# Kernel tuning notes

Measured on AMD Instinct MI355X. Metric: run time of the kernel, lower is better.

The kernel has to match this reference:

```python
import jax, jax.numpy as jnp
import numpy as np

N_NODES = 100000

def _sage_conv(x, src, dst, w_l, b_l, w_r):
    # PyG SAGEConv (mean aggr): out = lin_l(mean_j x_j) + lin_r(x_i)
    msg = x[src]                                             # [E, d] gather
    agg = jax.ops.segment_sum(msg, dst, num_segments=N_NODES)
    deg = jax.ops.segment_sum(jnp.ones((src.shape[0],), x.dtype), dst,
                              num_segments=N_NODES)
    mean = agg / jnp.maximum(deg, 1.0)[:, None]
    return mean @ w_l.T + b_l + x @ w_r.T


def setup_inputs() -> dict:
    key = jax.random.key(0)
    ks = jax.random.split(key, 9)
    d_in, d_h, d_out = 128, 128, 4
    E = 1600000
    x = jax.random.normal(ks[0], (N_NODES, d_in), dtype=jnp.float32)
    edge_index = jax.random.randint(ks[1], (2, E), 0, N_NODES, dtype=jnp.int32)
    s = lambda k, shp, fan: jax.random.normal(k, shp, jnp.float32) / np.sqrt(fan)
    return {
        "x": x,
        "edge_index": edge_index,
        "w1_l": s(ks[2], (d_h, d_in), d_in),
        "b1_l": jnp.zeros((d_h,), jnp.float32),
        "w1_r": s(ks[3], (d_h, d_in), d_in),
        "w2_l": s(ks[4], (d_h, d_h), d_h),
        "b2_l": jnp.zeros((d_h,), jnp.float32),
        "w2_r": s(ks[5], (d_h, d_h), d_h),
        "w_out": s(ks[6], (d_out, d_h), d_h),
        "b_out": jnp.zeros((d_out,), jnp.float32),
    }


def reference(x, edge_index, w1_l, b1_l, w1_r, w2_l, b2_l, w2_r, w_out, b_out):
    src, dst = edge_index[0], edge_index[1]
    h = jax.nn.relu(_sage_conv(x, src, dst, w1_l, b1_l, w1_r))
    h = jax.nn.relu(_sage_conv(h, src, dst, w2_l, b2_l, w2_r))
    return h @ w_out.T + b_out
```

## Files before the change

kernel.cpp:

```cpp
#include <hip/hip_runtime.h>

constexpr int D = 128;
constexpr int BSHIFT = 9;
constexpr int BNODES = 1 << BSHIFT;
constexpr int NBUCK_MAX = 256;
using short8 = __attribute__((ext_vector_type(8))) short;
using f32x4  = __attribute__((ext_vector_type(4))) float;

__device__ __forceinline__ unsigned rneb(float f) {
    unsigned u = __float_as_uint(f);
    return (u + 0x7fffu + ((u >> 16) & 1u)) >> 16;
}
__device__ __forceinline__ float lo2f(unsigned u) { return __uint_as_float(u << 16); }
__device__ __forceinline__ float hi2f(unsigned u) { return __uint_as_float(u & 0xffff0000u); }

__global__ __launch_bounds__(256) void misc_kernel(
    const float* __restrict__ w1l, const float* __restrict__ w1r,
    const float* __restrict__ w2l, const float* __restrict__ w2r,
    unsigned short* __restrict__ wf,
    const float* __restrict__ x, unsigned short* __restrict__ xb, int n4,
    int* __restrict__ bcnt)
{
    if (blockIdx.x < 32) {
        int t = blockIdx.x * 256 + threadIdx.x;
        int m = t >> 11;
        int r = t & 2047;
        int f = r >> 6, lane = r & 63;
        int c = f >> 2, ks = f & 3;
        int col = c * 16 + (lane & 15);
        int k0 = ks * 32 + (lane >> 4) * 8;
        const float* W = (m == 0) ? w1l : (m == 1) ? w1r : (m == 2) ? w2l : w2r;
        unsigned short o[8];
#pragma unroll
        for (int i = 0; i < 8; ++i) o[i] = (unsigned short)rneb(W[col * D + k0 + i]);
        uint4 pk;
        pk.x = o[0] | ((unsigned)o[1] << 16);
        pk.y = o[2] | ((unsigned)o[3] << 16);
        pk.z = o[4] | ((unsigned)o[5] << 16);
        pk.w = o[6] | ((unsigned)o[7] << 16);
        reinterpret_cast<uint4*>(wf)[t] = pk;
        return;
    }
    if (blockIdx.x == 32) bcnt[threadIdx.x] = 0;
    int i = (blockIdx.x - 32) * 256 + threadIdx.x;
    if (i >= n4) return;
    float4 v = reinterpret_cast<const float4*>(x)[i];
    uint2 o;
    o.x = rneb(v.x) | (rneb(v.y) << 16);
    o.y = rneb(v.z) | (rneb(v.w) << 16);
    reinterpret_cast<uint2*>(xb)[i] = o;
}

__global__ __launch_bounds__(256) void bucket_count(
    const int* __restrict__ dstI, int* __restrict__ bcnt, int E, int nb)
{
    __shared__ int lh[NBUCK_MAX];
    const int t = threadIdx.x;
    const int e0 = blockIdx.x * 4096;
    for (int i = t; i < nb; i += 256) lh[i] = 0;
    __syncthreads();
#pragma unroll
    for (int q = 0; q < 16; ++q) {
        int e = e0 + q * 256 + t;
        if (e < E) atomicAdd(&lh[dstI[e] >> BSHIFT], 1);
    }
    __syncthreads();
    for (int b = t; b < nb; b += 256)
        if (lh[b] > 0) atomicAdd(&bcnt[b], lh[b]);
}

__global__ __launch_bounds__(256) void bucket_scan(
    const int* __restrict__ bcnt, int* __restrict__ bbase,
    int* __restrict__ gcursor, int nb)
{
    __shared__ int tmp[256];
    const int t = threadIdx.x;
    const int v = (t < nb) ? bcnt[t] : 0;
    tmp[t] = v;
    __syncthreads();
    for (int off = 1; off < 256; off <<= 1) {
        int u = (t >= off) ? tmp[t - off] : 0;
        __syncthreads();
        tmp[t] += u;
        __syncthreads();
    }
    int excl = tmp[t] - v;
    if (t < nb) { bbase[t] = excl; gcursor[t] = excl; }
    if (t == nb - 1) bbase[nb] = excl + v;
}

__global__ __launch_bounds__(256) void bin_kernel(
    const int* __restrict__ srcI, const int* __restrict__ dstI,
    int* __restrict__ gcursor, unsigned* __restrict__ binned, int E, int nb)
{
    __shared__ int lhist[NBUCK_MAX];
    __shared__ int lbase[NBUCK_MAX];
    __shared__ int lcnt[NBUCK_MAX];
    const int t = threadIdx.x;
    const int e0 = blockIdx.x * 4096;
    for (int i = t; i < nb; i += 256) { lhist[i] = 0; lcnt[i] = 0; }
    __syncthreads();

    int dcache[16], scache[16];
#pragma unroll
    for (int q = 0; q < 16; ++q) {
        int e = e0 + q * 256 + t;
        int d = (e < E) ? dstI[e] : -1;
        dcache[q] = d;
        scache[q] = (e < E) ? srcI[e] : 0;
        if (d >= 0) atomicAdd(&lhist[d >> BSHIFT], 1);
    }
    __syncthreads();
    for (int b = t; b < nb; b += 256)
        if (lhist[b] > 0) lbase[b] = atomicAdd(&gcursor[b], lhist[b]);
    __syncthreads();
#pragma unroll
    for (int q = 0; q < 16; ++q) {
        int d = dcache[q];
        if (d >= 0) {
            int b = d >> BSHIFT;
            int off = atomicAdd(&lcnt[b], 1);
            binned[lbase[b] + off] =
                (unsigned)scache[q] | ((unsigned)(d & (BNODES - 1)) << 17);
        }
    }
}

__global__ __launch_bounds__(256) void bucket_build(
    const unsigned* __restrict__ binned, const int* __restrict__ bbase,
    int* __restrict__ rowptr, int* __restrict__ sorted_src, int n, int E)
{
    __shared__ int hist[BNODES];
    __shared__ int cur[BNODES];
    __shared__ int tmp[256];
    const int t = threadIdx.x;
    const int b = blockIdx.x;
    const int node0 = b << BSHIFT;
    const int ebeg = bbase[b];
    const int eend = bbase[b + 1];

    hist[t] = 0; hist[t + 256] = 0;
    __syncthreads();
    for (int e = ebeg + t; e < eend; e += 256)
        atomicAdd(&hist[(binned[e] >> 17) & (BNODES - 1)], 1);
    __syncthreads();

    const int v0 = hist[2 * t], v1 = hist[2 * t + 1];
    const int s = v0 + v1;
    tmp[t] = s;
    __syncthreads();
    for (int off = 1; off < 256; off <<= 1) {
        int u = (t >= off) ? tmp[t - off] : 0;
        __syncthreads();
        tmp[t] += u;
        __syncthreads();
    }
    const int pre = ebeg + tmp[t] - s;
    const int i0 = node0 + 2 * t, i1 = i0 + 1;
    cur[2 * t] = pre;
    cur[2 * t + 1] = pre + v0;
    if (i0 < n) rowptr[i0] = pre;
    if (i1 < n) rowptr[i1] = pre + v0;
    if (b == 0 && t == 0) rowptr[n] = E;
    __syncthreads();

    for (int e = ebeg + t; e < eend; e += 256) {
        unsigned w = binned[e];
        int pos = atomicAdd(&cur[(w >> 17) & (BNODES - 1)], 1);
        sorted_src[pos] = (int)(w & 0x1FFFF);
    }
}

__global__ __launch_bounds__(256) void aggregate_bf16(
    const unsigned short* __restrict__ feat, const int* __restrict__ sorted_src,
    const int* __restrict__ rowptr, unsigned short* __restrict__ outb, int n)
{
    const int wid = (blockIdx.x * 256 + threadIdx.x) >> 6;
    if (wid >= n) return;
    const int lane = threadIdx.x & 63;
    const int sub = lane >> 4;
    const int part = lane & 15;
    const int beg = rowptr[wid];
    const int end = rowptr[wid + 1];
    const int deg = end - beg;

    float acc[8];
#pragma unroll
    for (int j = 0; j < 8; ++j) acc[j] = 0.f;

    int e = beg;
    for (; e + 16 <= end; e += 16) {
        const int s0 = sorted_src[e + sub];
        const int s1 = sorted_src[e + 4 + sub];
        const int s2 = sorted_src[e + 8 + sub];
        const int s3 = sorted_src[e + 12 + sub];
        const uint4 v0 = *reinterpret_cast<const uint4*>(feat + (size_t)s0 * D + part * 8);
        const uint4 v1 = *reinterpret_cast<const uint4*>(feat + (size_t)s1 * D + part * 8);
        const uint4 v2 = *reinterpret_cast<const uint4*>(feat + (size_t)s2 * D + part * 8);
        const uint4 v3 = *reinterpret_cast<const uint4*>(feat + (size_t)s3 * D + part * 8);
        acc[0] += lo2f(v0.x); acc[1] += hi2f(v0.x);
        acc[2] += lo2f(v0.y); acc[3] += hi2f(v0.y);
        acc[4] += lo2f(v0.z); acc[5] += hi2f(v0.z);
        acc[6] += lo2f(v0.w); acc[7] += hi2f(v0.w);
        acc[0] += lo2f(v1.x); acc[1] += hi2f(v1.x);
        acc[2] += lo2f(v1.y); acc[3] += hi2f(v1.y);
        acc[4] += lo2f(v1.z); acc[5] += hi2f(v1.z);
        acc[6] += lo2f(v1.w); acc[7] += hi2f(v1.w);
        acc[0] += lo2f(v2.x); acc[1] += hi2f(v2.x);
        acc[2] += lo2f(v2.y); acc[3] += hi2f(v2.y);
        acc[4] += lo2f(v2.z); acc[5] += hi2f(v2.z);
        acc[6] += lo2f(v2.w); acc[7] += hi2f(v2.w);
        acc[0] += lo2f(v3.x); acc[1] += hi2f(v3.x);
        acc[2] += lo2f(v3.y); acc[3] += hi2f(v3.y);
        acc[4] += lo2f(v3.z); acc[5] += hi2f(v3.z);
        acc[6] += lo2f(v3.w); acc[7] += hi2f(v3.w);
    }
    if (e + 8 <= end) {
        const int s0 = sorted_src[e + sub];
        const int s1 = sorted_src[e + 4 + sub];
        const uint4 v0 = *reinterpret_cast<const uint4*>(feat + (size_t)s0 * D + part * 8);
        const uint4 v1 = *reinterpret_cast<const uint4*>(feat + (size_t)s1 * D + part * 8);
        acc[0] += lo2f(v0.x); acc[1] += hi2f(v0.x);
        acc[2] += lo2f(v0.y); acc[3] += hi2f(v0.y);
        acc[4] += lo2f(v0.z); acc[5] += hi2f(v0.z);
        acc[6] += lo2f(v0.w); acc[7] += hi2f(v0.w);
        acc[0] += lo2f(v1.x); acc[1] += hi2f(v1.x);
        acc[2] += lo2f(v1.y); acc[3] += hi2f(v1.y);
        acc[4] += lo2f(v1.z); acc[5] += hi2f(v1.z);
        acc[6] += lo2f(v1.w); acc[7] += hi2f(v1.w);
        e += 8;
    }
    if (e + 4 <= end) {
        const int s0 = sorted_src[e + sub];
        const uint4 v0 = *reinterpret_cast<const uint4*>(feat + (size_t)s0 * D + part * 8);
        acc[0] += lo2f(v0.x); acc[1] += hi2f(v0.x);
        acc[2] += lo2f(v0.y); acc[3] += hi2f(v0.y);
        acc[4] += lo2f(v0.z); acc[5] += hi2f(v0.z);
        acc[6] += lo2f(v0.w); acc[7] += hi2f(v0.w);
        e += 4;
    }
    if (e < end) {
        const int ei = e + sub;
        const bool act = ei < end;
        const int s = act ? sorted_src[ei] : sorted_src[beg];
        const float m = act ? 1.f : 0.f;
        const uint4 v = *reinterpret_cast<const uint4*>(feat + (size_t)s * D + part * 8);
        acc[0] += m * lo2f(v.x); acc[1] += m * hi2f(v.x);
        acc[2] += m * lo2f(v.y); acc[3] += m * hi2f(v.y);
        acc[4] += m * lo2f(v.z); acc[5] += m * hi2f(v.z);
        acc[6] += m * lo2f(v.w); acc[7] += m * hi2f(v.w);
    }

#pragma unroll
    for (int j = 0; j < 8; ++j) {
        acc[j] += __shfl_xor(acc[j], 16);
        acc[j] += __shfl_xor(acc[j], 32);
    }

    if (sub == 0) {
        const float inv = (deg > 0) ? 1.0f / (float)deg : 0.f;
        uint4 pk;
        pk.x = rneb(acc[0] * inv) | (rneb(acc[1] * inv) << 16);
        pk.y = rneb(acc[2] * inv) | (rneb(acc[3] * inv) << 16);
        pk.z = rneb(acc[4] * inv) | (rneb(acc[5] * inv) << 16);
        pk.w = rneb(acc[6] * inv) | (rneb(acc[7] * inv) << 16);
        *reinterpret_cast<uint4*>(outb + (size_t)wid * D + part * 8) = pk;
    }
}

__global__ __launch_bounds__(256) void mfma_gemm(
    const unsigned short* __restrict__ aMean, const unsigned short* __restrict__ aSelf,
    const unsigned short* __restrict__ wfL, const unsigned short* __restrict__ wfR,
    const float* __restrict__ bL, unsigned short* __restrict__ outb, int n)
{
    const int lane = threadIdx.x & 63;
    const int wave = threadIdx.x >> 6;
    const int lo = lane & 15, hi = lane >> 4;
    const int row0 = blockIdx.x * 64 + wave * 16;
    int arow = row0 + lo;
    if (arow > n - 1) arow = n - 1;
    const size_t abase = (size_t)arow * D;

    f32x4 acc[8];
#pragma unroll
    for (int c = 0; c < 8; ++c) acc[c] = (f32x4){0.f, 0.f, 0.f, 0.f};

#pragma unroll
    for (int p = 0; p < 2; ++p) {
        const unsigned short* A  = p ? aSelf : aMean;
        const unsigned short* WF = p ? wfR : wfL;
#pragma unroll
        for (int ks = 0; ks < 4; ++ks) {
            short8 af = *reinterpret_cast<const short8*>(A + abase + ks * 32 + hi * 8);
#pragma unroll
            for (int c = 0; c < 8; ++c) {
                short8 bf = *reinterpret_cast<const short8*>(
                    WF + ((((c << 2) | ks) * 64 + lane) << 3));
                acc[c] = __builtin_amdgcn_mfma_f32_16x16x32_bf16(af, bf, acc[c], 0, 0, 0);
            }
        }
    }

#pragma unroll
    for (int c = 0; c < 8; ++c) {
        const int col = (c << 4) | lo;
        const float bias = bL[col];
#pragma unroll
        for (int j = 0; j < 4; ++j) {
            const int row = row0 + (hi << 2) + j;
            if (row < n)
                outb[(size_t)row * D + col] =
                    (unsigned short)rneb(fmaxf(acc[c][j] + bias, 0.f));
        }
    }
}

__global__ __launch_bounds__(256) void mfma_gemm_out(
    const unsigned short* __restrict__ aMean, const unsigned short* __restrict__ aSelf,
    const unsigned short* __restrict__ wfL, const unsigned short* __restrict__ wfR,
    const float* __restrict__ bL, const float* __restrict__ w_out,
    const float* __restrict__ b_out, float* __restrict__ outp, int n)
{
    __shared__ float wsm[4 * D];
    wsm[threadIdx.x] = w_out[threadIdx.x];
    wsm[threadIdx.x + 256] = w_out[threadIdx.x + 256];
    __syncthreads();

    const int lane = threadIdx.x & 63;
    const int wave = threadIdx.x >> 6;
    const int lo = lane & 15, hi = lane >> 4;
    const int row0 = blockIdx.x * 64 + wave * 16;
    int arow = row0 + lo;
    if (arow > n - 1) arow = n - 1;
    const size_t abase = (size_t)arow * D;

    f32x4 acc[8];
#pragma unroll
    for (int c = 0; c < 8; ++c) acc[c] = (f32x4){0.f, 0.f, 0.f, 0.f};

#pragma unroll
    for (int p = 0; p < 2; ++p) {
        const unsigned short* A  = p ? aSelf : aMean;
        const unsigned short* WF = p ? wfR : wfL;
#pragma unroll
        for (int ks = 0; ks < 4; ++ks) {
            short8 af = *reinterpret_cast<const short8*>(A + abase + ks * 32 + hi * 8);
#pragma unroll
            for (int c = 0; c < 8; ++c) {
                short8 bf = *reinterpret_cast<const short8*>(
                    WF + ((((c << 2) | ks) * 64 + lane) << 3));
                acc[c] = __builtin_amdgcn_mfma_f32_16x16x32_bf16(af, bf, acc[c], 0, 0, 0);
            }
        }
    }

    float part[4][4];
#pragma unroll
    for (int j = 0; j < 4; ++j)
#pragma unroll
        for (int d = 0; d < 4; ++d) part[j][d] = 0.f;

#pragma unroll
    for (int c = 0; c < 8; ++c) {
        const int col = (c << 4) | lo;
        const float bias = bL[col];
        const float w0 = wsm[0 * D + col];
        const float w1 = wsm[1 * D + col];
        const float w2 = wsm[2 * D + col];
        const float w3 = wsm[3 * D + col];
#pragma unroll
        for (int j = 0; j < 4; ++j) {
            const float h = fmaxf(acc[c][j] + bias, 0.f);
            part[j][0] += h * w0;
            part[j][1] += h * w1;
            part[j][2] += h * w2;
            part[j][3] += h * w3;
        }
    }

#pragma unroll
    for (int m = 1; m < 16; m <<= 1) {
#pragma unroll
        for (int j = 0; j < 4; ++j)
#pragma unroll
            for (int d = 0; d < 4; ++d)
                part[j][d] += __shfl_xor(part[j][d], m);
    }

    if (lo == 0) {
        const float4 bo = *reinterpret_cast<const float4*>(b_out);
#pragma unroll
        for (int j = 0; j < 4; ++j) {
            const int row = row0 + (hi << 2) + j;
            if (row < n) {
                float4 o;
                o.x = part[j][0] + bo.x;
                o.y = part[j][1] + bo.y;
                o.z = part[j][2] + bo.z;
                o.w = part[j][3] + bo.w;
                *reinterpret_cast<float4*>(outp + (size_t)row * 4) = o;
            }
        }
    }
}

extern "C" void kernel_launch(void* const* d_in, const int* in_sizes, int n_in,
                              void* d_out, int out_size, void* d_ws, size_t ws_size,
                              hipStream_t stream)
{
    const float* x    = (const float*)d_in[0];
    const int*   ei   = (const int*)  d_in[1];
    const float* w1l  = (const float*)d_in[2];
    const float* b1l  = (const float*)d_in[3];
    const float* w1r  = (const float*)d_in[4];
    const float* w2l  = (const float*)d_in[5];
    const float* b2l  = (const float*)d_in[6];
    const float* w2r  = (const float*)d_in[7];
    const float* wout = (const float*)d_in[8];
    const float* bout = (const float*)d_in[9];

    const int n = in_sizes[0] / D;
    const int E = in_sizes[1] / 2;
    const int* srcI = ei;
    const int* dstI = ei + E;
    const int nbuck = (n + BNODES - 1) >> BSHIFT;

    auto align256 = [](size_t v) { return (v + 255) & ~(size_t)255; };
    char* base = (char*)d_ws;
    size_t off = 0;
    int* bcnt = (int*)(base + off);            off = align256(off + sizeof(int) * NBUCK_MAX);
    int* bbase = (int*)(base + off);           off = align256(off + sizeof(int) * (NBUCK_MAX + 1));
    int* gcursor = (int*)(base + off);         off = align256(off + sizeof(int) * NBUCK_MAX);
    int* rowptr = (int*)(base + off);          off = align256(off + sizeof(int) * (size_t)(n + 1));
    int* sorted_src = (int*)(base + off);      off = align256(off + sizeof(int) * (size_t)E);
    unsigned* binned = (unsigned*)(base + off); off = align256(off + sizeof(unsigned) * (size_t)E);
    unsigned short* xb = (unsigned short*)(base + off);
    off = align256(off + sizeof(short) * (size_t)n * D);
    unsigned short* bufA = (unsigned short*)(base + off);
    off = align256(off + sizeof(short) * (size_t)n * D);
    unsigned short* bufB = (unsigned short*)(base + off);
    off = align256(off + sizeof(short) * (size_t)n * D);
    unsigned short* wf = (unsigned short*)(base + off);

    const int n4 = n * (D / 4);
    const int cvtblocks = (n4 + 255) / 256;
    misc_kernel<<<32 + cvtblocks, 256, 0, stream>>>(w1l, w1r, w2l, w2r, wf,
                                                    x, xb, n4, bcnt);

    const int ebblocks = (E + 4095) / 4096;
    bucket_count<<<ebblocks, 256, 0, stream>>>(dstI, bcnt, E, nbuck);
    bucket_scan<<<1, 256, 0, stream>>>(bcnt, bbase, gcursor, nbuck);
    bin_kernel<<<ebblocks, 256, 0, stream>>>(srcI, dstI, gcursor, binned, E, nbuck);
    bucket_build<<<nbuck, 256, 0, stream>>>(binned, bbase, rowptr, sorted_src, n, E);

    const int ablocks = (int)(((long long)n * 64 + 255) / 256);
    const int gblocks = (n + 63) / 64;

    aggregate_bf16<<<ablocks, 256, 0, stream>>>(xb, sorted_src, rowptr, bufA, n);
    mfma_gemm<<<gblocks, 256, 0, stream>>>(bufA, xb, wf, wf + 16384, b1l, bufA, n);

    aggregate_bf16<<<ablocks, 256, 0, stream>>>(bufA, sorted_src, rowptr, bufB, n);
    mfma_gemm_out<<<gblocks, 256, 0, stream>>>(bufB, bufA, wf + 2 * 16384, wf + 3 * 16384,
                                               b2l, wout, bout, (float*)d_out, n);
}
```

Before: 353.7 us.

## Fuse neighbor-mean aggregation into the per-layer MFMA GEMM via LDS staging

Replaces the separate aggregate and GEMM kernels with one fused kernel per layer. Each wave computes the neighbor mean for 16 nodes, one node after another, and stages the bf16 results in padded shared memory. The MFMA GEMM then reads the mean operand from shared memory and the self operand from global memory. This removes the round trip of the mean buffer through global memory and two kernel launches. In exchange, each wave now gathers 16 nodes serially instead of one wave per node, which lowers the number of gathers in flight and can expose load imbalance across waves.

```diff
diff --git a/kernel.cpp b/kernel.cpp
--- a/kernel.cpp
+++ b/kernel.cpp
@@ -4,6 +4,7 @@
 constexpr int BSHIFT = 9;
 constexpr int BNODES = 1 << BSHIFT;
 constexpr int NBUCK_MAX = 256;
+constexpr int LP = 136;
 using short8 = __attribute__((ext_vector_type(8))) short;
 using f32x4  = __attribute__((ext_vector_type(4))) float;
 
@@ -171,115 +172,126 @@
     }
 }
 
-__global__ __launch_bounds__(256) void aggregate_bf16(
-    const unsigned short* __restrict__ feat, const int* __restrict__ sorted_src,
-    const int* __restrict__ rowptr, unsigned short* __restrict__ outb, int n)
-{
-    const int wid = (blockIdx.x * 256 + threadIdx.x) >> 6;
-    if (wid >= n) return;
+__global__ __launch_bounds__(256) void fused_layer(
+    const unsigned short* __restrict__ feat,
+    const int* __restrict__ sorted_src, const int* __restrict__ rowptr,
+    const unsigned short* __restrict__ wfL, const unsigned short* __restrict__ wfR,
+    const float* __restrict__ bL,
+    unsigned short* __restrict__ outb,
+    const float* __restrict__ w_out, const float* __restrict__ b_out,
+    float* __restrict__ outp,
+    int n, int mode)
+{
+    __shared__ unsigned short meanT[64 * LP];
+    __shared__ float wsm[4 * D];
+    wsm[threadIdx.x] = w_out[threadIdx.x];
+    wsm[threadIdx.x + 256] = w_out[threadIdx.x + 256];
+    __syncthreads();
+
+    const int wave = threadIdx.x >> 6;
     const int lane = threadIdx.x & 63;
-    const int sub = lane >> 4;
-    const int part = lane & 15;
-    const int beg = rowptr[wid];
-    const int end = rowptr[wid + 1];
-    const int deg = end - beg;
-
-    float acc[8];
-#pragma unroll
-    for (int j = 0; j < 8; ++j) acc[j] = 0.f;
-
-    int e = beg;
-    for (; e + 16 <= end; e += 16) {
-        const int s0 = sorted_src[e + sub];
-        const int s1 = sorted_src[e + 4 + sub];
-        const int s2 = sorted_src[e + 8 + sub];
-        const int s3 = sorted_src[e + 12 + sub];
-        const uint4 v0 = *reinterpret_cast<const uint4*>(feat + (size_t)s0 * D + part * 8);
-        const uint4 v1 = *reinterpret_cast<const uint4*>(feat + (size_t)s1 * D + part * 8);
-        const uint4 v2 = *reinterpret_cast<const uint4*>(feat + (size_t)s2 * D + part * 8);
-        const uint4 v3 = *reinterpret_cast<const uint4*>(feat + (size_t)s3 * D + part * 8);
-        acc[0] += lo2f(v0.x); acc[1] += hi2f(v0.x);
-        acc[2] += lo2f(v0.y); acc[3] += hi2f(v0.y);
-        acc[4] += lo2f(v0.z); acc[5] += hi2f(v0.z);
-        acc[6] += lo2f(v0.w); acc[7] += hi2f(v0.w);
-        acc[0] += lo2f(v1.x); acc[1] += hi2f(v1.x);
-        acc[2] += lo2f(v1.y); acc[3] += hi2f(v1.y);
-        acc[4] += lo2f(v1.z); acc[5] += hi2f(v1.z);
-        acc[6] += lo2f(v1.w); acc[7] += hi2f(v1.w);
-        acc[0] += lo2f(v2.x); acc[1] += hi2f(v2.x);
-        acc[2] += lo2f(v2.y); acc[3] += hi2f(v2.y);
-        acc[4] += lo2f(v2.z); acc[5] += hi2f(v2.z);
-        acc[6] += lo2f(v2.w); acc[7] += hi2f(v2.w);
-        acc[0] += lo2f(v3.x); acc[1] += hi2f(v3.x);
-        acc[2] += lo2f(v3.y); acc[3] += hi2f(v3.y);
-        acc[4] += lo2f(v3.z); acc[5] += hi2f(v3.z);
-        acc[6] += lo2f(v3.w); acc[7] += hi2f(v3.w);
-    }
-    if (e + 8 <= end) {
-        const int s0 = sorted_src[e + sub];
-        const int s1 = sorted_src[e + 4 + sub];
-        const uint4 v0 = *reinterpret_cast<const uint4*>(feat + (size_t)s0 * D + part * 8);
-        const uint4 v1 = *reinterpret_cast<const uint4*>(feat + (size_t)s1 * D + part * 8);
-        acc[0] += lo2f(v0.x); acc[1] += hi2f(v0.x);
-        acc[2] += lo2f(v0.y); acc[3] += hi2f(v0.y);
-        acc[4] += lo2f(v0.z); acc[5] += hi2f(v0.z);
-        acc[6] += lo2f(v0.w); acc[7] += hi2f(v0.w);
-        acc[0] += lo2f(v1.x); acc[1] += hi2f(v1.x);
-        acc[2] += lo2f(v1.y); acc[3] += hi2f(v1.y);
-        acc[4] += lo2f(v1.z); acc[5] += hi2f(v1.z);
-        acc[6] += lo2f(v1.w); acc[7] += hi2f(v1.w);
-        e += 8;
-    }
-    if (e + 4 <= end) {
-        const int s0 = sorted_src[e + sub];
-        const uint4 v0 = *reinterpret_cast<const uint4*>(feat + (size_t)s0 * D + part * 8);
-        acc[0] += lo2f(v0.x); acc[1] += hi2f(v0.x);
-        acc[2] += lo2f(v0.y); acc[3] += hi2f(v0.y);
-        acc[4] += lo2f(v0.z); acc[5] += hi2f(v0.z);
-        acc[6] += lo2f(v0.w); acc[7] += hi2f(v0.w);
-        e += 4;
-    }
-    if (e < end) {
-        const int ei = e + sub;
-        const bool act = ei < end;
-        const int s = act ? sorted_src[ei] : sorted_src[beg];
-        const float m = act ? 1.f : 0.f;
-        const uint4 v = *reinterpret_cast<const uint4*>(feat + (size_t)s * D + part * 8);
-        acc[0] += m * lo2f(v.x); acc[1] += m * hi2f(v.x);
-        acc[2] += m * lo2f(v.y); acc[3] += m * hi2f(v.y);
-        acc[4] += m * lo2f(v.z); acc[5] += m * hi2f(v.z);
-        acc[6] += m * lo2f(v.w); acc[7] += m * hi2f(v.w);
-    }
-
-#pragma unroll
-    for (int j = 0; j < 8; ++j) {
-        acc[j] += __shfl_xor(acc[j], 16);
-        acc[j] += __shfl_xor(acc[j], 32);
-    }
-
-    if (sub == 0) {
-        const float inv = (deg > 0) ? 1.0f / (float)deg : 0.f;
-        uint4 pk;
-        pk.x = rneb(acc[0] * inv) | (rneb(acc[1] * inv) << 16);
-        pk.y = rneb(acc[2] * inv) | (rneb(acc[3] * inv) << 16);
-        pk.z = rneb(acc[4] * inv) | (rneb(acc[5] * inv) << 16);
-        pk.w = rneb(acc[6] * inv) | (rneb(acc[7] * inv) << 16);
-        *reinterpret_cast<uint4*>(outb + (size_t)wid * D + part * 8) = pk;
-    }
-}
-
-__global__ __launch_bounds__(256) void mfma_gemm(
-    const unsigned short* __restrict__ aMean, const unsigned short* __restrict__ aSelf,
-    const unsigned short* __restrict__ wfL, const unsigned short* __restrict__ wfR,
-    const float* __restrict__ bL, unsigned short* __restrict__ outb, int n)
-{
-    const int lane = threadIdx.x & 63;
-    const int wave = threadIdx.x >> 6;
+    const int row0 = blockIdx.x * 64 + wave * 16;
+
+    {
+        const int sub = lane >> 4;
+        const int part = lane & 15;
+        for (int r = 0; r < 16; ++r) {
+            int node = row0 + r;
+            if (node > n - 1) node = n - 1;
+            const int beg = rowptr[node];
+            const int end = rowptr[node + 1];
+            const int deg = end - beg;
+
+            float acc[8];
+#pragma unroll
+            for (int j = 0; j < 8; ++j) acc[j] = 0.f;
+
+            int e = beg;
+            for (; e + 16 <= end; e += 16) {
+                const int s0 = sorted_src[e + sub];
+                const int s1 = sorted_src[e + 4 + sub];
+                const int s2 = sorted_src[e + 8 + sub];
+                const int s3 = sorted_src[e + 12 + sub];
+                const uint4 v0 = *reinterpret_cast<const uint4*>(feat + (size_t)s0 * D + part * 8);
+                const uint4 v1 = *reinterpret_cast<const uint4*>(feat + (size_t)s1 * D + part * 8);
+                const uint4 v2 = *reinterpret_cast<const uint4*>(feat + (size_t)s2 * D + part * 8);
+                const uint4 v3 = *reinterpret_cast<const uint4*>(feat + (size_t)s3 * D + part * 8);
+                acc[0] += lo2f(v0.x); acc[1] += hi2f(v0.x);
+                acc[2] += lo2f(v0.y); acc[3] += hi2f(v0.y);
+                acc[4] += lo2f(v0.z); acc[5] += hi2f(v0.z);
+                acc[6] += lo2f(v0.w); acc[7] += hi2f(v0.w);
+                acc[0] += lo2f(v1.x); acc[1] += hi2f(v1.x);
+                acc[2] += lo2f(v1.y); acc[3] += hi2f(v1.y);
+                acc[4] += lo2f(v1.z); acc[5] += hi2f(v1.z);
+                acc[6] += lo2f(v1.w); acc[7] += hi2f(v1.w);
+                acc[0] += lo2f(v2.x); acc[1] += hi2f(v2.x);
+                acc[2] += lo2f(v2.y); acc[3] += hi2f(v2.y);
+                acc[4] += lo2f(v2.z); acc[5] += hi2f(v2.z);
+                acc[6] += lo2f(v2.w); acc[7] += hi2f(v2.w);
+                acc[0] += lo2f(v3.x); acc[1] += hi2f(v3.x);
+                acc[2] += lo2f(v3.y); acc[3] += hi2f(v3.y);
+                acc[4] += lo2f(v3.z); acc[5] += hi2f(v3.z);
+                acc[6] += lo2f(v3.w); acc[7] += hi2f(v3.w);
+            }
+            if (e + 8 <= end) {
+                const int s0 = sorted_src[e + sub];
+                const int s1 = sorted_src[e + 4 + sub];
+                const uint4 v0 = *reinterpret_cast<const uint4*>(feat + (size_t)s0 * D + part * 8);
+                const uint4 v1 = *reinterpret_cast<const uint4*>(feat + (size_t)s1 * D + part * 8);
+                acc[0] += lo2f(v0.x); acc[1] += hi2f(v0.x);
+                acc[2] += lo2f(v0.y); acc[3] += hi2f(v0.y);
+                acc[4] += lo2f(v0.z); acc[5] += hi2f(v0.z);
+                acc[6] += lo2f(v0.w); acc[7] += hi2f(v0.w);
+                acc[0] += lo2f(v1.x); acc[1] += hi2f(v1.x);
+                acc[2] += lo2f(v1.y); acc[3] += hi2f(v1.y);
+                acc[4] += lo2f(v1.z); acc[5] += hi2f(v1.z);
+                acc[6] += lo2f(v1.w); acc[7] += hi2f(v1.w);
+                e += 8;
+            }
+            if (e + 4 <= end) {
+                const int s0 = sorted_src[e + sub];
+                const uint4 v0 = *reinterpret_cast<const uint4*>(feat + (size_t)s0 * D + part * 8);
+                acc[0] += lo2f(v0.x); acc[1] += hi2f(v0.x);
+                acc[2] += lo2f(v0.y); acc[3] += hi2f(v0.y);
+                acc[4] += lo2f(v0.z); acc[5] += hi2f(v0.z);
+                acc[6] += lo2f(v0.w); acc[7] += hi2f(v0.w);
+                e += 4;
+            }
+            if (e < end) {
+                const int ei = e + sub;
+                const bool act = ei < end;
+                const int s = act ? sorted_src[ei] : sorted_src[beg];
+                const float m = act ? 1.f : 0.f;
+                const uint4 v = *reinterpret_cast<const uint4*>(feat + (size_t)s * D + part * 8);
+                acc[0] += m * lo2f(v.x); acc[1] += m * hi2f(v.x);
+                acc[2] += m * lo2f(v.y); acc[3] += m * hi2f(v.y);
+                acc[4] += m * lo2f(v.z); acc[5] += m * hi2f(v.z);
+                acc[6] += m * lo2f(v.w); acc[7] += m * hi2f(v.w);
+            }
+
+#pragma unroll
+            for (int j = 0; j < 8; ++j) {
+                acc[j] += __shfl_xor(acc[j], 16);
+                acc[j] += __shfl_xor(acc[j], 32);
+            }
+
+            if (sub == 0) {
+                const float inv = (deg > 0) ? 1.0f / (float)deg : 0.f;
+                uint4 pk;
+                pk.x = rneb(acc[0] * inv) | (rneb(acc[1] * inv) << 16);
+                pk.y = rneb(acc[2] * inv) | (rneb(acc[3] * inv) << 16);
+                pk.z = rneb(acc[4] * inv) | (rneb(acc[5] * inv) << 16);
+                pk.w = rneb(acc[6] * inv) | (rneb(acc[7] * inv) << 16);
+                *reinterpret_cast<uint4*>(&meanT[(wave * 16 + r) * LP + part * 8]) = pk;
+            }
+        }
+    }
+
     const int lo = lane & 15, hi = lane >> 4;
-    const int row0 = blockIdx.x * 64 + wave * 16;
     int arow = row0 + lo;
     if (arow > n - 1) arow = n - 1;
     const size_t abase = (size_t)arow * D;
+    const unsigned short* ldsRow = &meanT[(wave * 16 + lo) * LP];
 
     f32x4 acc[8];
 #pragma unroll
@@ -287,11 +299,12 @@
 
 #pragma unroll
     for (int p = 0; p < 2; ++p) {
-        const unsigned short* A  = p ? aSelf : aMean;
         const unsigned short* WF = p ? wfR : wfL;
 #pragma unroll
         for (int ks = 0; ks < 4; ++ks) {
-            short8 af = *reinterpret_cast<const short8*>(A + abase + ks * 32 + hi * 8);
+            short8 af = p
+                ? *reinterpret_cast<const short8*>(feat + abase + ks * 32 + hi * 8)
+                : *reinterpret_cast<const short8*>(ldsRow + ks * 32 + hi * 8);
 #pragma unroll
             for (int c = 0; c < 8; ++c) {
                 short8 bf = *reinterpret_cast<const short8*>(
@@ -301,104 +314,66 @@
         }
     }
 
-#pragma unroll
-    for (int c = 0; c < 8; ++c) {
-        const int col = (c << 4) | lo;
-        const float bias = bL[col];
-#pragma unroll
-        for (int j = 0; j < 4; ++j) {
-            const int row = row0 + (hi << 2) + j;
-            if (row < n)
-                outb[(size_t)row * D + col] =
-                    (unsigned short)rneb(fmaxf(acc[c][j] + bias, 0.f));
-        }
-    }
-}
-
-__global__ __launch_bounds__(256) void mfma_gemm_out(
-    const unsigned short* __restrict__ aMean, const unsigned short* __restrict__ aSelf,
-    const unsigned short* __restrict__ wfL, const unsigned short* __restrict__ wfR,
-    const float* __restrict__ bL, const float* __restrict__ w_out,
-    const float* __restrict__ b_out, float* __restrict__ outp, int n)
-{
-    __shared__ float wsm[4 * D];
-    wsm[threadIdx.x] = w_out[threadIdx.x];
-    wsm[threadIdx.x + 256] = w_out[threadIdx.x + 256];
-    __syncthreads();
-
-    const int lane = threadIdx.x & 63;
-    const int wave = threadIdx.x >> 6;
-    const int lo = lane & 15, hi = lane >> 4;
-    const int row0 = blockIdx.x * 64 + wave * 16;
-    int arow = row0 + lo;
-    if (arow > n - 1) arow = n - 1;
-    const size_t abase = (size_t)arow * D;
-
-    f32x4 acc[8];
-#pragma unroll
-    for (int c = 0; c < 8; ++c) acc[c] = (f32x4){0.f, 0.f, 0.f, 0.f};
-
-#pragma unroll
-    for (int p = 0; p < 2; ++p) {
-        const unsigned short* A  = p ? aSelf : aMean;
-        const unsigned short* WF = p ? wfR : wfL;
-#pragma unroll
-        for (int ks = 0; ks < 4; ++ks) {
-            short8 af = *reinterpret_cast<const short8*>(A + abase + ks * 32 + hi * 8);
-#pragma unroll
-            for (int c = 0; c < 8; ++c) {
-                short8 bf = *reinterpret_cast<const short8*>(
-                    WF + ((((c << 2) | ks) * 64 + lane) << 3));
-                acc[c] = __builtin_amdgcn_mfma_f32_16x16x32_bf16(af, bf, acc[c], 0, 0, 0);
-            }
-        }
-    }
-
-    float part[4][4];
-#pragma unroll
-    for (int j = 0; j < 4; ++j)
-#pragma unroll
-        for (int d = 0; d < 4; ++d) part[j][d] = 0.f;
-
-#pragma unroll
-    for (int c = 0; c < 8; ++c) {
-        const int col = (c << 4) | lo;
-        const float bias = bL[col];
-        const float w0 = wsm[0 * D + col];
-        const float w1 = wsm[1 * D + col];
-        const float w2 = wsm[2 * D + col];
-        const float w3 = wsm[3 * D + col];
-#pragma unroll
-        for (int j = 0; j < 4; ++j) {
-            const float h = fmaxf(acc[c][j] + bias, 0.f);
-            part[j][0] += h * w0;
-            part[j][1] += h * w1;
-            part[j][2] += h * w2;
-            part[j][3] += h * w3;
-        }
-    }
-
-#pragma unroll
-    for (int m = 1; m < 16; m <<= 1) {
+    if (mode == 0) {
+#pragma unroll
+        for (int c = 0; c < 8; ++c) {
+            const int col = (c << 4) | lo;
+            const float bias = bL[col];
+#pragma unroll
+            for (int j = 0; j < 4; ++j) {
+                const int row = row0 + (hi << 2) + j;
+                if (row < n)
+                    outb[(size_t)row * D + col] =
+                        (unsigned short)rneb(fmaxf(acc[c][j] + bias, 0.f));
+            }
+        }
+    } else {
+        float part2[4][4];
 #pragma unroll
         for (int j = 0; j < 4; ++j)
 #pragma unroll
-            for (int d = 0; d < 4; ++d)
-                part[j][d] += __shfl_xor(part[j][d], m);
-    }
-
-    if (lo == 0) {
-        const float4 bo = *reinterpret_cast<const float4*>(b_out);
-#pragma unroll
-        for (int j = 0; j < 4; ++j) {
-            const int row = row0 + (hi << 2) + j;
-            if (row < n) {
-                float4 o;
-                o.x = part[j][0] + bo.x;
-                o.y = part[j][1] + bo.y;
-                o.z = part[j][2] + bo.z;
-                o.w = part[j][3] + bo.w;
-                *reinterpret_cast<float4*>(outp + (size_t)row * 4) = o;
+            for (int d = 0; d < 4; ++d) part2[j][d] = 0.f;
+
+#pragma unroll
+        for (int c = 0; c < 8; ++c) {
+            const int col = (c << 4) | lo;
+            const float bias = bL[col];
+            const float w0 = wsm[0 * D + col];
+            const float w1 = wsm[1 * D + col];
+            const float w2 = wsm[2 * D + col];
+            const float w3 = wsm[3 * D + col];
+#pragma unroll
+            for (int j = 0; j < 4; ++j) {
+                const float h = fmaxf(acc[c][j] + bias, 0.f);
+                part2[j][0] += h * w0;
+                part2[j][1] += h * w1;
+                part2[j][2] += h * w2;
+                part2[j][3] += h * w3;
+            }
+        }
+
+#pragma unroll
+        for (int m = 1; m < 16; m <<= 1) {
+#pragma unroll
+            for (int j = 0; j < 4; ++j)
+#pragma unroll
+                for (int d = 0; d < 4; ++d)
+                    part2[j][d] += __shfl_xor(part2[j][d], m);
+        }
+
+        if (lo == 0) {
+            const float4 bo = *reinterpret_cast<const float4*>(b_out);
+#pragma unroll
+            for (int j = 0; j < 4; ++j) {
+                const int row = row0 + (hi << 2) + j;
+                if (row < n) {
+                    float4 o;
+                    o.x = part2[j][0] + bo.x;
+                    o.y = part2[j][1] + bo.y;
+                    o.z = part2[j][2] + bo.z;
+                    o.w = part2[j][3] + bo.w;
+                    *reinterpret_cast<float4*>(outp + (size_t)row * 4) = o;
+                }
             }
         }
     }
@@ -438,8 +413,6 @@
     off = align256(off + sizeof(short) * (size_t)n * D);
     unsigned short* bufA = (unsigned short*)(base + off);
     off = align256(off + sizeof(short) * (size_t)n * D);
-    unsigned short* bufB = (unsigned short*)(base + off);
-    off = align256(off + sizeof(short) * (size_t)n * D);
     unsigned short* wf = (unsigned short*)(base + off);
 
     const int n4 = n * (D / 4);
@@ -453,13 +426,13 @@
     bin_kernel<<<ebblocks, 256, 0, stream>>>(srcI, dstI, gcursor, binned, E, nbuck);
     bucket_build<<<nbuck, 256, 0, stream>>>(binned, bbase, rowptr, sorted_src, n, E);
 
-    const int ablocks = (int)(((long long)n * 64 + 255) / 256);
     const int gblocks = (n + 63) / 64;
 
-    aggregate_bf16<<<ablocks, 256, 0, stream>>>(xb, sorted_src, rowptr, bufA, n);
-    mfma_gemm<<<gblocks, 256, 0, stream>>>(bufA, xb, wf, wf + 16384, b1l, bufA, n);
-
-    aggregate_bf16<<<ablocks, 256, 0, stream>>>(bufA, sorted_src, rowptr, bufB, n);
-    mfma_gemm_out<<<gblocks, 256, 0, stream>>>(bufB, bufA, wf + 2 * 16384, wf + 3 * 16384,
-                                               b2l, wout, bout, (float*)d_out, n);
-}
+    fused_layer<<<gblocks, 256, 0, stream>>>(
+        xb, sorted_src, rowptr, wf, wf + 16384, b1l,
+        bufA, wout, bout, nullptr, n, 0);
+
+    fused_layer<<<gblocks, 256, 0, stream>>>(
+        bufA, sorted_src, rowptr, wf + 2 * 16384, wf + 3 * 16384, b2l,
+        nullptr, wout, bout, (float*)d_out, n, 1);
+}
```

Result: slower. 451.0 us (+27.5%).
